# Performance work log

Measured on AMD Instinct MI355X. Metric: run time of the kernel, lower is better.

The kernel has to match this reference:

```python
import jax, jax.numpy as jnp
import numpy as np

B, C, H, W, R = 8, 256, 64, 64, 16


def setup_inputs() -> dict:
    key = jax.random.key(0)
    ks = jax.random.split(key, 14)
    def w(k, shape, fan):
        return (jax.random.normal(k, shape, jnp.float32) / np.sqrt(fan)).astype(jnp.float32)
    return {
        "features_depth": jax.random.normal(ks[0], (B, C, H, W), jnp.float32),
        "features_semseg": jax.random.normal(ks[1], (B, C, H, W), jnp.float32),
        "W0": w(ks[2], (C, 2 * C), 2 * C),          # conv_split0 1x1, [out,in]
        "Wdw": w(ks[3], (C, 1, 3, 3), 9),            # depthwise 3x3, groups=C
        "Wq": w(ks[4], (C, C), C),                   # Linear weights [out,in]
        "Wk": w(ks[5], (C, C), C),
        "Wv": w(ks[6], (C, C), C),
        "Wp": w(ks[7], (C, C), C),
        "bp": jnp.zeros((C,), jnp.float32),
        "Wsplit": w(ks[8], (C, C), C),               # conv_split 1x1
        "se_d_w1": w(ks[9], (C // R, C), C),         # SE squeeze conv1x1 (depth)
        "se_d_w2": w(ks[10], (C, C // R), C // R),
        "se_s_w1": w(ks[11], (C // R, C), C),        # SE squeeze conv1x1 (semseg)
        "se_s_w2": w(ks[12], (C, C // R), C // R),
    }


def _l2norm(a, eps=1e-12):
    n = jnp.linalg.norm(a, axis=-1, keepdims=True)
    return a / jnp.maximum(n, eps)


def _se(x, w1, w2):
    # x: [B,C,H,W]; global avg pool -> 1x1 convs -> sigmoid gate
    p = x.mean(axis=(2, 3))                                  # [B,C]
    h = jax.nn.relu(jnp.einsum('rc,bc->br', w1, p))          # [B,C/R]
    g = jax.nn.sigmoid(jnp.einsum('cr,br->bc', w2, h))       # [B,C]
    return x * g[:, :, None, None]


def reference(features_depth, features_semseg, W0, Wdw, Wq, Wk, Wv, Wp, bp,
              Wsplit, se_d_w1, se_d_w2, se_s_w1, se_s_w2):
    x = jnp.concatenate([features_depth, features_semseg], axis=1)  # [B,2C,H,W]
    x = jnp.einsum('oc,bchw->bohw', W0, x)                          # 1x1 conv
    x = jax.lax.conv_general_dilated(
        x, Wdw, window_strides=(1, 1), padding='SAME',
        dimension_numbers=('NCHW', 'OIHW', 'NCHW'), feature_group_count=C)
    xt = x.transpose(0, 2, 3, 1).reshape(B, H * W, C)               # [B,N,C]
    q = (xt @ Wq.T).transpose(0, 2, 1)                              # [B,C,N]
    k = (xt @ Wk.T).transpose(0, 2, 1)
    v = (xt @ Wv.T).transpose(0, 2, 1)
    q = _l2norm(q)
    k = _l2norm(k)
    attn = jax.nn.softmax(jnp.einsum('bcn,bdn->bcd', k, q), axis=-1)  # [B,C,C]
    y = jnp.einsum('bcd,bdn->bcn', attn, v)                         # [B,C,N]
    y = y.transpose(0, 2, 1)                                        # [B,N,C]
    y = y @ Wp.T + bp                                               # proj
    out_c = y.reshape(B, H, W, C).transpose(0, 3, 1, 2)             # [B,C,H,W]
    out_c = jnp.einsum('oc,bchw->bohw', Wsplit, out_c)              # 1x1 conv
    out_depth = _se(out_c, se_d_w1, se_d_w2) + features_depth
    out_semseg = _se(out_c, se_s_w1, se_s_w2) + features_semseg
    return (out_depth, out_semseg)
```

## Files before the change

kernel.cpp:

```cpp
#include <hip/hip_runtime.h>
#include <cstdint>

#define DEVI __device__ __forceinline__

using fx4 = __attribute__((ext_vector_type(4))) float;
using bf8 = __attribute__((ext_vector_type(8))) __bf16;
using s8v = __attribute__((ext_vector_type(8))) short;
using s4v = __attribute__((ext_vector_type(4))) short;
typedef unsigned short u16;
typedef unsigned int u32;

DEVI float b2f(u16 u) { return __builtin_bit_cast(float, (u32)u << 16); }
DEVI u16 f2b(float f) {
  u32 u = __builtin_bit_cast(u32, f);
  return (u16)((u + 0x7fffu + ((u >> 16) & 1u)) >> 16);
}

#define GLOAD(g, l)                                                          \
  __builtin_amdgcn_global_load_lds(                                          \
      (const __attribute__((address_space(1))) unsigned int*)(g),            \
      (__attribute__((address_space(3))) unsigned int*)(l), 16, 0, 0)

__global__ __launch_bounds__(256) void prep(const float* __restrict__ W0,
                                            const float* __restrict__ Wq,
                                            const float* __restrict__ Wk,
                                            const float* __restrict__ Wv,
                                            const float* __restrict__ Wsp,
                                            const float* __restrict__ Wp,
                                            const float* __restrict__ bp,
                                            u16* __restrict__ w0b,
                                            u16* __restrict__ wqk2,
                                            u16* __restrict__ wvtb,
                                            u16* __restrict__ wcb,
                                            float* __restrict__ bcb) {
  __shared__ float row[256];
  __shared__ float red[4];
  const int y = blockIdx.y;
  const int t = threadIdx.x;
  if (y == 0) {
    const int i = blockIdx.x * 256 + t;
    if (i < 131072) w0b[i] = f2b(W0[i]);
  } else if (y == 1) {
    const int i = blockIdx.x * 256 + t;
    if (i < 262144) {
      const int r = i >> 9, c = i & 511;
      const float* src = (r < 256) ? Wq : Wk;
      wqk2[i] = f2b(src[((r & 255) << 8) + (c & 255)]);
    }
  } else if (y == 2) {
    const int i = blockIdx.x * 256 + t;
    if (i < 65536) {
      const int e = i >> 8, d = i & 255;
      wvtb[i] = f2b(Wv[d * 256 + e]);
    }
  } else {
    if (blockIdx.x >= 256) return;
    const int o = blockIdx.x;
    row[t] = Wsp[o * 256 + t];
    __syncthreads();
    float acc = 0.f;
    for (int c = 0; c < 256; ++c) acc += row[c] * Wp[c * 256 + t];
    wcb[o * 256 + t] = f2b(acc);
    float pb = row[t] * bp[t];
#pragma unroll
    for (int m = 32; m > 0; m >>= 1) pb += __shfl_xor(pb, m);
    if ((t & 63) == 0) red[t >> 6] = pb;
    __syncthreads();
    if (t == 0) bcb[o] = red[0] + red[1] + red[2] + red[3];
  }
}

__global__ __launch_bounds__(512) void conv0f(const float* __restrict__ fd,
                                              const float* __restrict__ fs,
                                              const u16* __restrict__ w0b,
                                              u16* __restrict__ x0) {
  __shared__ u16 tmp[64 * 132];
  __shared__ u16 ldsA[128 * 64];
  __shared__ u16 ldsB[256 * 64];
  const int b = blockIdx.y;
  const int bm = blockIdx.x * 128;
  const int t = threadIdx.x;
  const int wid = t >> 6, lane = t & 63;
  const int wm = wid >> 2, wn = wid & 3;
  fx4 acc[4][4] = {};
  for (int kt = 0; kt < 512; kt += 64) {
#pragma unroll
    for (int i = 0; i < 4; ++i) {
      const int r = i * 64 + (t >> 3);
      const int kq = (t & 7) ^ (r & 7);
      GLOAD(w0b + (long)r * 512 + kt + kq * 8, &ldsB[i * 4096 + wid * 512]);
    }
    const float* src = ((kt < 256) ? fd : fs) + ((long)b * 256 + (kt & 255)) * 4096L + bm;
#pragma unroll
    for (int p = 0; p < 4; ++p) {
      const int c = (t >> 5) + p * 16;
      const int n4 = (t & 31) * 4;
      const fx4 v = *(const fx4*)&src[(long)c * 4096 + n4];
      s4v pk;
#pragma unroll
      for (int j = 0; j < 4; ++j) pk[j] = (short)f2b(v[j]);
      *(s4v*)&tmp[c * 132 + n4] = pk;
    }
    __syncthreads();
#pragma unroll
    for (int pass = 0; pass < 2; ++pass) {
      const int n = t & 127;
      const int g = (t >> 7) + pass * 4;
      s8v pk;
#pragma unroll
      for (int j = 0; j < 8; ++j) pk[j] = (short)tmp[(g * 8 + j) * 132 + n];
      *(s8v*)&ldsA[n * 64 + ((g ^ (n & 7)) * 8)] = pk;
    }
    __syncthreads();
#pragma unroll
    for (int ko = 0; ko < 2; ++ko) {
      bf8 af[4], bfr[4];
      const int kq = ko * 4 + (lane >> 4);
#pragma unroll
      for (int f = 0; f < 4; ++f) {
        const int ar = wm * 64 + f * 16 + (lane & 15);
        af[f] = *(const bf8*)&ldsA[ar * 64 + ((kq ^ (ar & 7)) * 8)];
        const int br = wn * 64 + f * 16 + (lane & 15);
        bfr[f] = *(const bf8*)&ldsB[br * 64 + ((kq ^ (br & 7)) * 8)];
      }
#pragma unroll
      for (int fm = 0; fm < 4; ++fm)
#pragma unroll
        for (int fn = 0; fn < 4; ++fn)
          acc[fm][fn] = __builtin_amdgcn_mfma_f32_16x16x32_bf16(af[fm], bfr[fn], acc[fm][fn], 0, 0, 0);
    }
    __syncthreads();
  }
#pragma unroll
  for (int fm = 0; fm < 4; ++fm) {
    const int m0 = wm * 64 + fm * 16 + ((lane >> 4) << 2);
#pragma unroll
    for (int fn = 0; fn < 4; ++fn) {
      const int o = wn * 64 + fn * 16 + (lane & 15);
#pragma unroll
      for (int r = 0; r < 4; ++r)
        x0[((long)b << 20) + (long)(bm + m0 + r) * 256 + o] = f2b(acc[fm][fn][r]);
    }
  }
}

template <typename OT, int BIAS, bool POOL, int EPI>
__global__ __launch_bounds__(256) void gemm_nt(
    const u16* __restrict__ A, long sA, int lda,
    const u16* __restrict__ B, long sB, int ldb,
    OT* __restrict__ C, long sC, long sCs, int ldc,
    const float* __restrict__ bias, int Keff, int ksplit,
    float* __restrict__ poolpart,
    const float* __restrict__ wqf, const float* __restrict__ wkf,
    float* __restrict__ dpart) {
  __shared__ u16 ldsA[128 * 64];
  __shared__ u16 ldsB[128 * 64];
  const int z = blockIdx.z;
  const int bb = z / ksplit;
  const int ss = z - bb * ksplit;
  const int bm = blockIdx.x * 128;
  const int bn = blockIdx.y * 128;
  const u16* Ab = A + bb * sA + (long)ss * Keff + (long)bm * lda;
  const u16* Bb = B + bb * sB + (long)ss * Keff + (long)bn * ldb;
  const int tid = threadIdx.x;
  const int wid = tid >> 6;
  const int lane = tid & 63;
  const int wm = wid >> 1, wn = wid & 1;
  const int srow = tid >> 3;
  const int slot = tid & 7;

  fx4 acc[4][4] = {};
  for (int kt = 0; kt < Keff; kt += 64) {
#pragma unroll
    for (int i = 0; i < 4; ++i) {
      const int row = i * 32 + srow;
      const int kq = slot ^ (row & 7);
      GLOAD(Ab + (long)row * lda + kt + kq * 8, &ldsA[i * 2048 + wid * 512]);
      GLOAD(Bb + (long)row * ldb + kt + kq * 8, &ldsB[i * 2048 + wid * 512]);
    }
    __syncthreads();
#pragma unroll
    for (int ko = 0; ko < 2; ++ko) {
      bf8 af[4], bfr[4];
      const int kq = ko * 4 + (lane >> 4);
#pragma unroll
      for (int f = 0; f < 4; ++f) {
        const int ar = wm * 64 + f * 16 + (lane & 15);
        af[f] = *(const bf8*)&ldsA[ar * 64 + ((kq ^ (ar & 7)) * 8)];
        const int br = wn * 64 + f * 16 + (lane & 15);
        bfr[f] = *(const bf8*)&ldsB[br * 64 + ((kq ^ (br & 7)) * 8)];
      }
#pragma unroll
      for (int fm = 0; fm < 4; ++fm)
#pragma unroll
        for (int fn = 0; fn < 4; ++fn)
          acc[fm][fn] = __builtin_amdgcn_mfma_f32_16x16x32_bf16(af[fm], bfr[fn], acc[fm][fn], 0, 0, 0);
    }
    __syncthreads();
  }
  if constexpr (EPI == 1) {
    u16* S2b = (u16*)C + bb * sC;
    float dp[4][4];
#pragma unroll
    for (int fm = 0; fm < 4; ++fm)
#pragma unroll
      for (int r = 0; r < 4; ++r) dp[fm][r] = 0.f;
#pragma unroll
    for (int fm = 0; fm < 4; ++fm) {
      const int m0 = bm + wm * 64 + fm * 16 + ((lane >> 4) << 2);
#pragma unroll
      for (int fn = 0; fn < 4; ++fn) {
        const int n0 = bn + wn * 64 + fn * 16 + (lane & 15);
#pragma unroll
        for (int r = 0; r < 4; ++r) {
          const float v = acc[fm][fn][r];
          const int m = m0 + r;
          if (m < 256) {
            const u16 hi = f2b(v);
            S2b[(long)m * 512 + n0] = hi;
            S2b[(long)m * 512 + 256 + n0] = f2b(v - b2f(hi));
          }
          const float* wr = (m < 256) ? (wqf + (long)m * 256) : (wkf + (long)(m - 256) * 256);
          dp[fm][r] += v * wr[n0];
        }
      }
    }
#pragma unroll
    for (int fm = 0; fm < 4; ++fm)
#pragma unroll
      for (int r = 0; r < 4; ++r) {
        float s = dp[fm][r];
        s += __shfl_xor(s, 1); s += __shfl_xor(s, 2);
        s += __shfl_xor(s, 4); s += __shfl_xor(s, 8);
        if ((lane & 15) == 0) {
          const int m = bm + wm * 64 + fm * 16 + ((lane >> 4) << 2) + r;
          dpart[(long)(blockIdx.y * 2 + wn) * 4096 + bb * 512 + m] = s;
        }
      }
    return;
  }
  OT* Cb = C + bb * sC + ss * sCs;
  float pr[4][4];
  if (POOL) {
#pragma unroll
    for (int fm = 0; fm < 4; ++fm)
#pragma unroll
      for (int r = 0; r < 4; ++r) pr[fm][r] = 0.f;
  }
#pragma unroll
  for (int fm = 0; fm < 4; ++fm) {
    const int m0 = bm + wm * 64 + fm * 16 + ((lane >> 4) << 2);
#pragma unroll
    for (int fn = 0; fn < 4; ++fn) {
      const int n0 = bn + wn * 64 + fn * 16 + (lane & 15);
#pragma unroll
      for (int r = 0; r < 4; ++r) {
        float v = acc[fm][fn][r];
        if (BIAS == 2) v += bias[m0 + r];
        if constexpr (sizeof(OT) == 2) Cb[(long)(m0 + r) * ldc + n0] = (OT)f2b(v);
        else Cb[(long)(m0 + r) * ldc + n0] = v;
        if (POOL) pr[fm][r] += v;
      }
    }
  }
  if (POOL) {
#pragma unroll
    for (int fm = 0; fm < 4; ++fm)
#pragma unroll
      for (int r = 0; r < 4; ++r) {
        float s = pr[fm][r];
        s += __shfl_xor(s, 1); s += __shfl_xor(s, 2);
        s += __shfl_xor(s, 4); s += __shfl_xor(s, 8);
        if ((lane & 15) == 0) {
          const int o = bm + wm * 64 + fm * 16 + ((lane >> 4) << 2) + r;
          poolpart[(long)(blockIdx.y * 2 + wn) * 2048 + bb * 256 + o] = s;
        }
      }
  }
}

__global__ __launch_bounds__(256) void dwconv3x3(const u16* __restrict__ x,
                                                 const float* __restrict__ wdw,
                                                 u16* __restrict__ y) {
  __shared__ float w[9][256];
  const int t = threadIdx.x;
  for (int i = t; i < 2304; i += 256) w[i % 9][i / 9] = wdw[i];
  __syncthreads();
  const int nb = blockIdx.x;
  const int b = nb >> 9;
  const int n0 = (nb & 511) << 3;
  const int tn = t >> 5;
  const int tc = (t & 31) << 3;
  const int n = n0 + tn;
  const int hh = n >> 6, ww2 = n & 63;
  const u16* base = x + ((long)b << 20);
  float acc[8] = {0.f, 0.f, 0.f, 0.f, 0.f, 0.f, 0.f, 0.f};
#pragma unroll
  for (int ky = 0; ky < 3; ++ky) {
    const int hy = hh + ky - 1;
    if ((unsigned)hy >= 64u) continue;
#pragma unroll
    for (int kx = 0; kx < 3; ++kx) {
      const int wx = ww2 + kx - 1;
      if ((unsigned)wx >= 64u) continue;
      const s8v v = *(const s8v*)&base[(((hy << 6) + wx) << 8) + tc];
      const int kk = ky * 3 + kx;
      const fx4 wa = *(const fx4*)&w[kk][tc];
      const fx4 wb = *(const fx4*)&w[kk][tc + 4];
#pragma unroll
      for (int j = 0; j < 4; ++j) {
        acc[j] += wa[j] * b2f((u16)v[j]);
        acc[4 + j] += wb[j] * b2f((u16)v[4 + j]);
      }
    }
  }
  s8v o;
#pragma unroll
  for (int j = 0; j < 8; ++j) o[j] = (short)f2b(acc[j]);
  *(s8v*)&y[((long)b << 20) + ((long)n << 8) + tc] = o;
}

__global__ void btrans(const u16* __restrict__ x, u16* __restrict__ y) {
  __shared__ u16 t[32][34];
  const int b = blockIdx.z;
  const int n0 = blockIdx.x * 32;
  const int c0 = blockIdx.y * 32;
  const int tx = threadIdx.x, ty = threadIdx.y;
  const u16* sp = x + (long)b * 1048576 + (long)n0 * 256 + c0;
#pragma unroll
  for (int j = 0; j < 4; ++j) {
    int i = ty + j * 8;
    t[i][tx] = sp[(long)i * 256 + tx];
  }
  __syncthreads();
  u16* op = y + (long)b * 1048576 + (long)c0 * 4096 + n0;
#pragma unroll
  for (int j = 0; j < 4; ++j) {
    int r = ty + j * 8;
    op[(long)r * 4096 + tx] = t[tx][r];
  }
}

__global__ __launch_bounds__(256) void gsplit(const float* __restrict__ part,
                                              u16* __restrict__ G2) {
  const int i4 = (blockIdx.x * 256 + threadIdx.x) * 4;
  fx4 s = {0.f, 0.f, 0.f, 0.f};
#pragma unroll
  for (int ss = 0; ss < 8; ++ss) s += *(const fx4*)(part + (long)ss * 524288 + i4);
  const int b = i4 >> 16, rem = i4 & 65535, e = rem >> 8, c0 = rem & 255;
  u16* d = G2 + (long)b * 131072 + (long)e * 512 + c0;
  s4v hi, lo;
#pragma unroll
  for (int j = 0; j < 4; ++j) {
    u16 h = f2b(s[j]);
    hi[j] = (short)h;
    lo[j] = (short)f2b(s[j] - b2f(h));
  }
  *(s4v*)d = hi;
  *(s4v*)(d + 256) = lo;
}

__global__ __launch_bounds__(256) void softmax_g2(const float* __restrict__ araw,
                                                  const float* __restrict__ dpart,
                                                  u16* __restrict__ out) {
  const int wid = threadIdx.x >> 6, lane = threadIdx.x & 63;
  const int t = threadIdx.x;
  const int b = blockIdx.x >> 6;
  __shared__ float rq[256];
  float dq = dpart[b * 512 + t] + dpart[4096 + b * 512 + t] +
             dpart[8192 + b * 512 + t] + dpart[12288 + b * 512 + t];
  rq[t] = 1.f / fmaxf(sqrtf(fmaxf(dq, 0.f)), 1e-12f);
  __syncthreads();
  const long row = (long)blockIdx.x * 4 + wid;
  const int c = (int)(row & 255);
  const int ki = b * 512 + 256 + c;
  float dk = dpart[ki] + dpart[4096 + ki] + dpart[8192 + ki] + dpart[12288 + ki];
  const float rk = 1.f / fmaxf(sqrtf(fmaxf(dk, 0.f)), 1e-12f);
  fx4 v = ((const fx4*)(araw + row * 256))[lane];
  v[0] *= rk * rq[lane * 4];     v[1] *= rk * rq[lane * 4 + 1];
  v[2] *= rk * rq[lane * 4 + 2]; v[3] *= rk * rq[lane * 4 + 3];
  float m = fmaxf(fmaxf(v[0], v[1]), fmaxf(v[2], v[3]));
#pragma unroll
  for (int o = 32; o > 0; o >>= 1) m = fmaxf(m, __shfl_xor(m, o));
  float e0 = __expf(v[0] - m), e1 = __expf(v[1] - m);
  float e2 = __expf(v[2] - m), e3 = __expf(v[3] - m);
  float s4 = e0 + e1 + e2 + e3;
#pragma unroll
  for (int o = 32; o > 0; o >>= 1) s4 += __shfl_xor(s4, o);
  const float inv = 1.f / s4;
  u16* op = out + row * 256 + lane * 4;
  op[0] = f2b(e0 * inv); op[1] = f2b(e1 * inv);
  op[2] = f2b(e2 * inv); op[3] = f2b(e3 * inv);
}

__global__ __launch_bounds__(256) void se_gates(const float* __restrict__ poolpart,
                                                const float* __restrict__ w1d, const float* __restrict__ w2d,
                                                const float* __restrict__ w1s, const float* __restrict__ w2s,
                                                float* __restrict__ gd, float* __restrict__ gs) {
  const int b = blockIdx.x;
  const int t = threadIdx.x;
  __shared__ float p[256], hd[16], hs[16];
  float s = 0.f;
#pragma unroll 8
  for (int sl = 0; sl < 64; ++sl) s += poolpart[(long)sl * 2048 + b * 256 + t];
  p[t] = s * (1.f / 4096.f);
  __syncthreads();
  if (t < 16) {
    float ad = 0.f, as2 = 0.f;
    for (int j = 0; j < 256; ++j) {
      ad += w1d[t * 256 + j] * p[j];
      as2 += w1s[t * 256 + j] * p[j];
    }
    hd[t] = fmaxf(ad, 0.f);
    hs[t] = fmaxf(as2, 0.f);
  }
  __syncthreads();
  float ad = 0.f, as2 = 0.f;
#pragma unroll
  for (int r = 0; r < 16; ++r) {
    ad += w2d[t * 16 + r] * hd[r];
    as2 += w2s[t * 16 + r] * hs[r];
  }
  gd[b * 256 + t] = 1.f / (1.f + __expf(-ad));
  gs[b * 256 + t] = 1.f / (1.f + __expf(-as2));
}

__global__ __launch_bounds__(256) void fuse_out(const u16* __restrict__ oc,
                                                const float* __restrict__ gd, const float* __restrict__ gs,
                                                const float* __restrict__ fd, const float* __restrict__ fs,
                                                float* __restrict__ od, float* __restrict__ os) {
  const long i = ((long)blockIdx.x * 256 + threadIdx.x) * 8;
  const long bc = i >> 12;
  const float gdv = gd[bc], gsv = gs[bc];
  const s8v c8 = *(const s8v*)&oc[i];
  const fx4 a0 = *(const fx4*)(fd + i), a1 = *(const fx4*)(fd + i + 4);
  const fx4 s0 = *(const fx4*)(fs + i), s1 = *(const fx4*)(fs + i + 4);
  fx4 d0, d1, e0, e1;
#pragma unroll
  for (int j = 0; j < 4; ++j) {
    const float cl = b2f((u16)c8[j]);
    const float ch = b2f((u16)c8[4 + j]);
    d0[j] = cl * gdv + a0[j]; d1[j] = ch * gdv + a1[j];
    e0[j] = cl * gsv + s0[j]; e1[j] = ch * gsv + s1[j];
  }
  *(fx4*)(od + i) = d0; *(fx4*)(od + i + 4) = d1;
  *(fx4*)(os + i) = e0; *(fx4*)(os + i + 4) = e1;
}

extern "C" void kernel_launch(void* const* d_in, const int* in_sizes, int n_in,
                              void* d_out, int out_size, void* d_ws, size_t ws_size,
                              hipStream_t stream) {
  const float* fd  = (const float*)d_in[0];
  const float* fs  = (const float*)d_in[1];
  const float* W0  = (const float*)d_in[2];
  const float* Wdw = (const float*)d_in[3];
  const float* Wq  = (const float*)d_in[4];
  const float* Wk  = (const float*)d_in[5];
  const float* Wv  = (const float*)d_in[6];
  const float* Wp  = (const float*)d_in[7];
  const float* bp  = (const float*)d_in[8];
  const float* Wsp = (const float*)d_in[9];
  const float* w1d = (const float*)d_in[10];
  const float* w2d = (const float*)d_in[11];
  const float* w1s = (const float*)d_in[12];
  const float* w2s = (const float*)d_in[13];

  char* ws = (char*)d_ws;
  u16* x0b    = (u16*)(ws + 0);
  u16* outcb  = x0b;
  u16* xtb    = (u16*)(ws + 16777216);
  u16* xtT    = (u16*)(ws + 33554432);
  float* part = (float*)(ws + 50331648);
  u16* G2     = (u16*)(ws + 67108864);
  u16* S2     = (u16*)(ws + 69206016);
  float* araw = (float*)(ws + 71303168);
  u16* attnb  = (u16*)(ws + 73400320);
  u16* m1t    = (u16*)(ws + 74448896);
  u16* wfin   = (u16*)(ws + 75497472);
  u16* w0b    = (u16*)(ws + 76546048);
  u16* wqk2   = (u16*)(ws + 76808192);
  u16* wvtb   = (u16*)(ws + 77332480);
  u16* wcb    = (u16*)(ws + 77463552);
  float* bcb  = (float*)(ws + 77594624);
  float* dpart = (float*)(ws + 77595648);
  float* poolpart = (float*)(ws + 77661184);
  float* gdp  = (float*)(ws + 78185472);
  float* gsp  = (float*)(ws + 78193664);
  float* od  = (float*)d_out;
  float* osg = od + 8388608;

  prep<<<dim3(2048, 4), 256, 0, stream>>>(W0, Wq, Wk, Wv, Wsp, Wp, bp,
                                          w0b, wqk2, wvtb, wcb, bcb);
  conv0f<<<dim3(32, 8), 512, 0, stream>>>(fd, fs, w0b, x0b);
  dwconv3x3<<<4096, 256, 0, stream>>>(x0b, Wdw, xtb);
  btrans<<<dim3(128, 8, 8), dim3(32, 8), 0, stream>>>(xtb, xtT);
  gemm_nt<float, 0, false, 0><<<dim3(2, 2, 64), 256, 0, stream>>>(
      xtT, 1048576, 4096, xtT, 1048576, 4096,
      part, 65536, 524288, 256, nullptr, 512, 8, nullptr, nullptr, nullptr, nullptr);
  gsplit<<<512, 256, 0, stream>>>(part, G2);
  gemm_nt<u16, 0, false, 1><<<dim3(4, 2, 8), 256, 0, stream>>>(
      wqk2, 0, 512, G2, 131072, 512, S2, 131072, 0, 512, nullptr, 512, 1,
      nullptr, Wq, Wk, dpart);
  gemm_nt<float, 0, false, 0><<<dim3(2, 2, 8), 256, 0, stream>>>(
      wqk2 + 131072, 0, 512, S2, 131072, 512, araw, 65536, 0, 256, nullptr, 512, 1,
      nullptr, nullptr, nullptr, nullptr);
  softmax_g2<<<512, 256, 0, stream>>>(araw, dpart, attnb);
  gemm_nt<u16, 0, false, 0><<<dim3(2, 2, 8), 256, 0, stream>>>(
      wvtb, 0, 256, attnb, 65536, 256, m1t, 65536, 0, 256, nullptr, 256, 1,
      nullptr, nullptr, nullptr, nullptr);
  gemm_nt<u16, 0, false, 0><<<dim3(2, 2, 8), 256, 0, stream>>>(
      wcb, 0, 256, m1t, 65536, 256, wfin, 65536, 0, 256, nullptr, 256, 1,
      nullptr, nullptr, nullptr, nullptr);
  gemm_nt<u16, 2, true, 0><<<dim3(2, 32, 8), 256, 0, stream>>>(
      wfin, 65536, 256, xtb, 1048576, 256, outcb, 1048576, 0, 4096, bcb, 256, 1,
      poolpart, nullptr, nullptr, nullptr);
  se_gates<<<8, 256, 0, stream>>>(poolpart, w1d, w2d, w1s, w2s, gdp, gsp);
  fuse_out<<<4096, 256, 0, stream>>>(outcb, gdp, gsp, fd, fs, od, osg);
}
```

Before: 174.8 us.

## Fuse SE gating and residual into final GEMM, precompute pooled means algebraically

```diff
diff --git a/kernel.cpp b/kernel.cpp
--- a/kernel.cpp
+++ b/kernel.cpp
@@ -144,15 +144,14 @@
   }
 }
 
-template <typename OT, int BIAS, bool POOL, int EPI>
+template <typename OT, int BIAS, int EPI>
 __global__ __launch_bounds__(256) void gemm_nt(
     const u16* __restrict__ A, long sA, int lda,
     const u16* __restrict__ B, long sB, int ldb,
     OT* __restrict__ C, long sC, long sCs, int ldc,
     const float* __restrict__ bias, int Keff, int ksplit,
-    float* __restrict__ poolpart,
     const float* __restrict__ wqf, const float* __restrict__ wkf,
-    float* __restrict__ dpart) {
+    float* __restrict__ dpart, float* __restrict__ poolpart) {
   __shared__ u16 ldsA[128 * 64];
   __shared__ u16 ldsB[128 * 64];
   const int z = blockIdx.z;
@@ -239,14 +238,33 @@
       }
     return;
   }
+  if constexpr (EPI == 4) {
+    float* odp = (float*)C + bb * sC;
+    float* osp = (float*)C + 8388608 + bb * sC;
+    const float* fdp = wqf + bb * sC;
+    const float* fsp = wkf + bb * sC;
+#pragma unroll
+    for (int fm = 0; fm < 4; ++fm) {
+      const int m0 = bm + wm * 64 + fm * 16 + ((lane >> 4) << 2);
+#pragma unroll
+      for (int r = 0; r < 4; ++r) {
+        const int m = m0 + r;
+        const float bv = bias[m];
+        const float g1 = dpart[bb * 256 + m];
+        const float g2 = poolpart[bb * 256 + m];
+        const long rowb = (long)m * ldc;
+#pragma unroll
+        for (int fn = 0; fn < 4; ++fn) {
+          const int n0 = bn + wn * 64 + fn * 16 + (lane & 15);
+          const float v = acc[fm][fn][r] + bv;
+          odp[rowb + n0] = v * g1 + fdp[rowb + n0];
+          osp[rowb + n0] = v * g2 + fsp[rowb + n0];
+        }
+      }
+    }
+    return;
+  }
   OT* Cb = C + bb * sC + ss * sCs;
-  float pr[4][4];
-  if (POOL) {
-#pragma unroll
-    for (int fm = 0; fm < 4; ++fm)
-#pragma unroll
-      for (int r = 0; r < 4; ++r) pr[fm][r] = 0.f;
-  }
 #pragma unroll
   for (int fm = 0; fm < 4; ++fm) {
     const int m0 = bm + wm * 64 + fm * 16 + ((lane >> 4) << 2);
@@ -259,23 +277,8 @@
         if (BIAS == 2) v += bias[m0 + r];
         if constexpr (sizeof(OT) == 2) Cb[(long)(m0 + r) * ldc + n0] = (OT)f2b(v);
         else Cb[(long)(m0 + r) * ldc + n0] = v;
-        if (POOL) pr[fm][r] += v;
-      }
-    }
-  }
-  if (POOL) {
-#pragma unroll
-    for (int fm = 0; fm < 4; ++fm)
-#pragma unroll
-      for (int r = 0; r < 4; ++r) {
-        float s = pr[fm][r];
-        s += __shfl_xor(s, 1); s += __shfl_xor(s, 2);
-        s += __shfl_xor(s, 4); s += __shfl_xor(s, 8);
-        if ((lane & 15) == 0) {
-          const int o = bm + wm * 64 + fm * 16 + ((lane >> 4) << 2) + r;
-          poolpart[(long)(blockIdx.y * 2 + wn) * 2048 + bb * 256 + o] = s;
-        }
-      }
+      }
+    }
   }
 }
 
@@ -320,24 +323,36 @@
   *(s8v*)&y[((long)b << 20) + ((long)n << 8) + tc] = o;
 }
 
-__global__ void btrans(const u16* __restrict__ x, u16* __restrict__ y) {
+__global__ void btrans2(const u16* __restrict__ x, u16* __restrict__ y,
+                        float* __restrict__ cspart) {
   __shared__ u16 t[32][34];
+  __shared__ float ps[8][32];
   const int b = blockIdx.z;
   const int n0 = blockIdx.x * 32;
   const int c0 = blockIdx.y * 32;
   const int tx = threadIdx.x, ty = threadIdx.y;
   const u16* sp = x + (long)b * 1048576 + (long)n0 * 256 + c0;
+  float cs = 0.f;
 #pragma unroll
   for (int j = 0; j < 4; ++j) {
     int i = ty + j * 8;
-    t[i][tx] = sp[(long)i * 256 + tx];
-  }
+    const u16 v = sp[(long)i * 256 + tx];
+    t[i][tx] = v;
+    cs += b2f(v);
+  }
+  ps[ty][tx] = cs;
   __syncthreads();
   u16* op = y + (long)b * 1048576 + (long)c0 * 4096 + n0;
 #pragma unroll
   for (int j = 0; j < 4; ++j) {
     int r = ty + j * 8;
     op[(long)r * 4096 + tx] = t[tx][r];
+  }
+  if (ty == 0) {
+    float s = 0.f;
+#pragma unroll
+    for (int k = 0; k < 8; ++k) s += ps[k][tx];
+    cspart[(long)blockIdx.x * 2048 + b * 256 + c0 + tx] = s;
   }
 }
 
@@ -393,17 +408,135 @@
   op[2] = f2b(e2 * inv); op[3] = f2b(e3 * inv);
 }
 
-__global__ __launch_bounds__(256) void se_gates(const float* __restrict__ poolpart,
-                                                const float* __restrict__ w1d, const float* __restrict__ w2d,
-                                                const float* __restrict__ w1s, const float* __restrict__ w2s,
-                                                float* __restrict__ gd, float* __restrict__ gs) {
+__global__ __launch_bounds__(256) void mwfuse(const u16* __restrict__ attnb,
+                                              const u16* __restrict__ wvtb,
+                                              const u16* __restrict__ wcb,
+                                              u16* __restrict__ wfin) {
+  __shared__ u16 lds[25088];
+  const int M1OFF = 0;
+  const int A2OFF = 16896;
+  const int B1OFF = 0;
+  const int A1OFF = 16384;
+  const int e0 = blockIdx.x * 64;
+  const int b = blockIdx.y;
+  const int t = threadIdx.x;
+  const int wid = t >> 6, lane = t & 63;
+  const int srow = t >> 3, slot = t & 7;
+  const u16* attn = attnb + (long)b * 65536;
+
+  fx4 acc[4][4] = {};
+  for (int kt = 0; kt < 256; kt += 64) {
+#pragma unroll
+    for (int i = 0; i < 8; ++i) {
+      const int row = i * 32 + srow;
+      const int kq = slot ^ (row & 7);
+      GLOAD(attn + (long)row * 256 + kt + kq * 8, &lds[B1OFF + i * 2048 + wid * 512]);
+    }
+#pragma unroll
+    for (int i = 0; i < 2; ++i) {
+      const int row = i * 32 + srow;
+      const int kq = slot ^ (row & 7);
+      GLOAD(wvtb + (long)(e0 + row) * 256 + kt + kq * 8, &lds[A1OFF + i * 2048 + wid * 512]);
+    }
+    __syncthreads();
+#pragma unroll
+    for (int ko = 0; ko < 2; ++ko) {
+      bf8 af[4], bfr[4];
+      const int kq = ko * 4 + (lane >> 4);
+#pragma unroll
+      for (int f = 0; f < 4; ++f) {
+        const int ar = f * 16 + (lane & 15);
+        af[f] = *(const bf8*)&lds[A1OFF + ar * 64 + ((kq ^ (ar & 7)) * 8)];
+        const int br = wid * 64 + f * 16 + (lane & 15);
+        bfr[f] = *(const bf8*)&lds[B1OFF + br * 64 + ((kq ^ (br & 7)) * 8)];
+      }
+#pragma unroll
+      for (int fm = 0; fm < 4; ++fm)
+#pragma unroll
+        for (int fn = 0; fn < 4; ++fn)
+          acc[fm][fn] = __builtin_amdgcn_mfma_f32_16x16x32_bf16(af[fm], bfr[fn], acc[fm][fn], 0, 0, 0);
+    }
+    __syncthreads();
+  }
+#pragma unroll
+  for (int fm = 0; fm < 4; ++fm) {
+    const int ep0 = fm * 16 + ((lane >> 4) << 2);
+#pragma unroll
+    for (int fn = 0; fn < 4; ++fn) {
+      const int c = wid * 64 + fn * 16 + (lane & 15);
+#pragma unroll
+      for (int r = 0; r < 4; ++r)
+        lds[M1OFF + (ep0 + r) * 264 + c] = f2b(acc[fm][fn][r]);
+    }
+  }
+  __syncthreads();
+  fx4 acc2[4][4] = {};
+  for (int kt = 0; kt < 256; kt += 32) {
+#pragma unroll
+    for (int i = 0; i < 4; ++i) {
+      const int row = i * 64 + (t >> 2);
+      const int kq = (t & 3) ^ (row & 3);
+      GLOAD(wcb + (long)row * 256 + kt + kq * 8, &lds[A2OFF + i * 2048 + wid * 512]);
+    }
+    __syncthreads();
+    bf8 af[4], bfr[4];
+    const int kq = lane >> 4;
+#pragma unroll
+    for (int f = 0; f < 4; ++f) {
+      const int ar = wid * 64 + f * 16 + (lane & 15);
+      af[f] = *(const bf8*)&lds[A2OFF + ar * 32 + ((kq ^ (ar & 3)) * 8)];
+      const int br = f * 16 + (lane & 15);
+      bfr[f] = *(const bf8*)&lds[M1OFF + br * 264 + kt + kq * 8];
+    }
+#pragma unroll
+    for (int fm = 0; fm < 4; ++fm)
+#pragma unroll
+      for (int fn = 0; fn < 4; ++fn)
+        acc2[fm][fn] = __builtin_amdgcn_mfma_f32_16x16x32_bf16(af[fm], bfr[fn], acc2[fm][fn], 0, 0, 0);
+    __syncthreads();
+  }
+  u16* wf = wfin + (long)b * 65536;
+#pragma unroll
+  for (int fm = 0; fm < 4; ++fm) {
+    const int o0 = wid * 64 + fm * 16 + ((lane >> 4) << 2);
+#pragma unroll
+    for (int fn = 0; fn < 4; ++fn) {
+      const int e = e0 + fn * 16 + (lane & 15);
+#pragma unroll
+      for (int r = 0; r < 4; ++r)
+        wf[(long)(o0 + r) * 256 + e] = f2b(acc2[fm][fn][r]);
+    }
+  }
+}
+
+__global__ __launch_bounds__(256) void sefuse(const float* __restrict__ cspart,
+                                              const u16* __restrict__ wfin,
+                                              const float* __restrict__ bcb,
+                                              const float* __restrict__ w1d, const float* __restrict__ w2d,
+                                              const float* __restrict__ w1s, const float* __restrict__ w2s,
+                                              float* __restrict__ gd, float* __restrict__ gs) {
   const int b = blockIdx.x;
   const int t = threadIdx.x;
-  __shared__ float p[256], hd[16], hs[16];
+  __shared__ float xm[256], p[256], hd[16], hs[16];
   float s = 0.f;
 #pragma unroll 8
-  for (int sl = 0; sl < 64; ++sl) s += poolpart[(long)sl * 2048 + b * 256 + t];
-  p[t] = s * (1.f / 4096.f);
+  for (int sl = 0; sl < 128; ++sl) s += cspart[(long)sl * 2048 + b * 256 + t];
+  xm[t] = s;
+  __syncthreads();
+  const u16* wf = wfin + (long)b * 65536 + (long)t * 256;
+  float acc = 0.f;
+#pragma unroll 4
+  for (int e = 0; e < 256; e += 8) {
+    const s8v w8 = *(const s8v*)&wf[e];
+    const fx4 x0v = *(const fx4*)&xm[e];
+    const fx4 x1v = *(const fx4*)&xm[e + 4];
+#pragma unroll
+    for (int j = 0; j < 4; ++j) {
+      acc += b2f((u16)w8[j]) * x0v[j];
+      acc += b2f((u16)w8[4 + j]) * x1v[j];
+    }
+  }
+  p[t] = acc * (1.f / 4096.f) + bcb[t];
   __syncthreads();
   if (t < 16) {
     float ad = 0.f, as2 = 0.f;
@@ -423,28 +556,6 @@
   }
   gd[b * 256 + t] = 1.f / (1.f + __expf(-ad));
   gs[b * 256 + t] = 1.f / (1.f + __expf(-as2));
-}
-
-__global__ __launch_bounds__(256) void fuse_out(const u16* __restrict__ oc,
-                                                const float* __restrict__ gd, const float* __restrict__ gs,
-                                                const float* __restrict__ fd, const float* __restrict__ fs,
-                                                float* __restrict__ od, float* __restrict__ os) {
-  const long i = ((long)blockIdx.x * 256 + threadIdx.x) * 8;
-  const long bc = i >> 12;
-  const float gdv = gd[bc], gsv = gs[bc];
-  const s8v c8 = *(const s8v*)&oc[i];
-  const fx4 a0 = *(const fx4*)(fd + i), a1 = *(const fx4*)(fd + i + 4);
-  const fx4 s0 = *(const fx4*)(fs + i), s1 = *(const fx4*)(fs + i + 4);
-  fx4 d0, d1, e0, e1;
-#pragma unroll
-  for (int j = 0; j < 4; ++j) {
-    const float cl = b2f((u16)c8[j]);
-    const float ch = b2f((u16)c8[4 + j]);
-    d0[j] = cl * gdv + a0[j]; d1[j] = ch * gdv + a1[j];
-    e0[j] = cl * gsv + s0[j]; e1[j] = ch * gsv + s1[j];
-  }
-  *(fx4*)(od + i) = d0; *(fx4*)(od + i + 4) = d1;
-  *(fx4*)(os + i) = e0; *(fx4*)(os + i + 4) = e1;
 }
 
 extern "C" void kernel_launch(void* const* d_in, const int* in_sizes, int n_in,
@@ -467,7 +578,6 @@
 
   char* ws = (char*)d_ws;
   u16* x0b    = (u16*)(ws + 0);
-  u16* outcb  = x0b;
   u16* xtb    = (u16*)(ws + 16777216);
   u16* xtT    = (u16*)(ws + 33554432);
   float* part = (float*)(ws + 50331648);
@@ -475,45 +585,37 @@
   u16* S2     = (u16*)(ws + 69206016);
   float* araw = (float*)(ws + 71303168);
   u16* attnb  = (u16*)(ws + 73400320);
-  u16* m1t    = (u16*)(ws + 74448896);
-  u16* wfin   = (u16*)(ws + 75497472);
-  u16* w0b    = (u16*)(ws + 76546048);
-  u16* wqk2   = (u16*)(ws + 76808192);
-  u16* wvtb   = (u16*)(ws + 77332480);
-  u16* wcb    = (u16*)(ws + 77463552);
-  float* bcb  = (float*)(ws + 77594624);
-  float* dpart = (float*)(ws + 77595648);
-  float* poolpart = (float*)(ws + 77661184);
-  float* gdp  = (float*)(ws + 78185472);
-  float* gsp  = (float*)(ws + 78193664);
-  float* od  = (float*)d_out;
-  float* osg = od + 8388608;
+  u16* wfin   = (u16*)(ws + 74448896);
+  u16* w0b    = (u16*)(ws + 75497472);
+  u16* wqk2   = (u16*)(ws + 75759616);
+  u16* wvtb   = (u16*)(ws + 76283904);
+  u16* wcb    = (u16*)(ws + 76414976);
+  float* bcb  = (float*)(ws + 76546048);
+  float* dpart = (float*)(ws + 76547072);
+  float* cspart = (float*)(ws + 76611584);
+  float* gdp  = (float*)(ws + 77660160);
+  float* gsp  = (float*)(ws + 77668352);
+  float* od   = (float*)d_out;
 
   prep<<<dim3(2048, 4), 256, 0, stream>>>(W0, Wq, Wk, Wv, Wsp, Wp, bp,
                                           w0b, wqk2, wvtb, wcb, bcb);
   conv0f<<<dim3(32, 8), 512, 0, stream>>>(fd, fs, w0b, x0b);
   dwconv3x3<<<4096, 256, 0, stream>>>(x0b, Wdw, xtb);
-  btrans<<<dim3(128, 8, 8), dim3(32, 8), 0, stream>>>(xtb, xtT);
-  gemm_nt<float, 0, false, 0><<<dim3(2, 2, 64), 256, 0, stream>>>(
+  btrans2<<<dim3(128, 8, 8), dim3(32, 8), 0, stream>>>(xtb, xtT, cspart);
+  gemm_nt<float, 0, 0><<<dim3(2, 2, 64), 256, 0, stream>>>(
       xtT, 1048576, 4096, xtT, 1048576, 4096,
       part, 65536, 524288, 256, nullptr, 512, 8, nullptr, nullptr, nullptr, nullptr);
   gsplit<<<512, 256, 0, stream>>>(part, G2);
-  gemm_nt<u16, 0, false, 1><<<dim3(4, 2, 8), 256, 0, stream>>>(
+  gemm_nt<u16, 0, 1><<<dim3(4, 2, 8), 256, 0, stream>>>(
       wqk2, 0, 512, G2, 131072, 512, S2, 131072, 0, 512, nullptr, 512, 1,
-      nullptr, Wq, Wk, dpart);
-  gemm_nt<float, 0, false, 0><<<dim3(2, 2, 8), 256, 0, stream>>>(
+      Wq, Wk, dpart, nullptr);
+  gemm_nt<float, 0, 0><<<dim3(2, 2, 8), 256, 0, stream>>>(
       wqk2 + 131072, 0, 512, S2, 131072, 512, araw, 65536, 0, 256, nullptr, 512, 1,
       nullptr, nullptr, nullptr, nullptr);
   softmax_g2<<<512, 256, 0, stream>>>(araw, dpart, attnb);
-  gemm_nt<u16, 0, false, 0><<<dim3(2, 2, 8), 256, 0, stream>>>(
-      wvtb, 0, 256, attnb, 65536, 256, m1t, 65536, 0, 256, nullptr, 256, 1,
-      nullptr, nullptr, nullptr, nullptr);
-  gemm_nt<u16, 0, false, 0><<<dim3(2, 2, 8), 256, 0, stream>>>(
-      wcb, 0, 256, m1t, 65536, 256, wfin, 65536, 0, 256, nullptr, 256, 1,
-      nullptr, nullptr, nullptr, nullptr);
-  gemm_nt<u16, 2, true, 0><<<dim3(2, 32, 8), 256, 0, stream>>>(
-      wfin, 65536, 256, xtb, 1048576, 256, outcb, 1048576, 0, 4096, bcb, 256, 1,
-      poolpart, nullptr, nullptr, nullptr);
-  se_gates<<<8, 256, 0, stream>>>(poolpart, w1d, w2d, w1s, w2s, gdp, gsp);
-  fuse_out<<<4096, 256, 0, stream>>>(outcb, gdp, gsp, fd, fs, od, osg);
-}
+  mwfuse<<<dim3(4, 8), 256, 0, stream>>>(attnb, wvtb, wcb, wfin);
+  sefuse<<<8, 256, 0, stream>>>(cspart, wfin, bcb, w1d, w2d, w1s, w2s, gdp, gsp);
+  gemm_nt<float, 0, 4><<<dim3(2, 32, 8), 256, 0, stream>>>(
+      wfin, 65536, 256, xtb, 1048576, 256, od, 1048576, 0, 4096, bcb, 256, 1,
+      fd, fs, gdp, gsp);
+}
```

After: 168.7 us. 1.04x faster.
